# Performance work log

Hardware: AMD Instinct MI355X
Metric: run time of the kernel (lower is better)

## Reference

```python
import jax, jax.numpy as jnp
import numpy as np

BATCH = 8
NDATA = 8192
NPOINT = 1024
NSAMPLE = 32
RADIUS = 0.2
CFEAT = 64


def setup_inputs() -> dict:
    key = jax.random.key(0)
    k1, k2, k3 = jax.random.split(key, 3)
    new_xyz = jax.random.normal(k1, (BATCH, NPOINT, 3), dtype=jnp.float32)
    xyz = jax.random.normal(k2, (BATCH, NDATA, 3), dtype=jnp.float32)
    points = jax.random.normal(k3, (BATCH, NDATA, CFEAT), dtype=jnp.float32)
    return {"new_xyz": new_xyz, "xyz": xyz, "points": points}


def reference(new_xyz, xyz, points):
    # Pairwise distances from every centroid to every dataset point.
    # delta: [B, P, N, 3]
    delta = xyz[:, None, :, :] - new_xyz[:, :, None, :]
    dist = jnp.linalg.norm(delta, axis=-1)  # [B, P, N]

    # Sort by distance (the original does a full argsort per centroid).
    sorted_idx = jnp.argsort(dist, axis=-1).astype(jnp.int32)  # [B, P, N]
    sorted_d = jnp.take_along_axis(dist, sorted_idx, axis=-1)  # [B, P, N]

    # Nearest point index replaces out-of-radius slots.
    nearest = sorted_idx[:, :, 0:1]  # [B, P, 1]
    radius_idx = jnp.where(sorted_d < RADIUS, sorted_idx, nearest)
    idx = radius_idx[:, :, :NSAMPLE]  # [B, P, S] int32 (ndataset >= nsample)

    # Batched gathers: grouped_xyz [B, P, S, 3], grouped_points [B, P, S, C].
    grouped_xyz = jnp.take_along_axis(
        xyz[:, None, :, :], idx[..., None], axis=2)
    grouped_points = jnp.take_along_axis(
        points[:, None, :, :], idx[..., None], axis=2)
    new_points = jnp.concatenate([grouped_xyz, grouped_points], axis=-1)
    return (new_points, idx, grouped_xyz)
```

## Files before the change

### kernel.cpp

```cpp
#include <hip/hip_runtime.h>
#include <math.h>

typedef unsigned int   u32;
typedef unsigned long long u64;

#define BATCH   8
#define NDATA   8192
#define NPOINT  1024
#define NSAMPLE 32
#define CFEAT   64
#define ROWF    67
#define MAXCAND 128
#define QPB     4
#define NB      256

#define OUT_IDX (BATCH*NPOINT*NSAMPLE*ROWF)
#define OUT_GX  (OUT_IDX + BATCH*NPOINT*NSAMPLE)

__device__ __forceinline__ float rnbf(float f) {
    u32 b = __float_as_uint(f);
    b += 0x7FFFu + ((b >> 16) & 1u);
    return __uint_as_float(b & 0xFFFF0000u);
}
__device__ __forceinline__ int clampidx(int v) {
    return (v < 0) ? 0 : (v > NDATA-1 ? NDATA-1 : v);
}
__device__ __forceinline__ int lanes_below(u64 m) {
    return __builtin_amdgcn_mbcnt_hi((u32)(m >> 32),
            __builtin_amdgcn_mbcnt_lo((u32)m, 0));
}
__device__ __forceinline__ int xbucket(float v) {
    int c = (int)floorf((v + 4.5f) * 28.444445f);
    return c < 0 ? 0 : (c > NB-1 ? NB-1 : c);
}

__global__ __launch_bounds__(1024)
void bin_kernel(const float* __restrict__ xyz,
                float4* __restrict__ wp, u32* __restrict__ wst)
{
    __shared__ u32 cnt[NB];
    __shared__ u32 sc[NB];
    const int b = blockIdx.x, tid = threadIdx.x;
    const float* bx = xyz + (size_t)b * NDATA * 3;

    if (tid < NB) cnt[tid] = 0;
    __syncthreads();
    for (int p = tid; p < NDATA; p += 1024)
        atomicAdd(&cnt[xbucket(bx[p*3])], 1u);
    __syncthreads();

    if (tid < NB) sc[tid] = cnt[tid];
    __syncthreads();
    #pragma unroll
    for (int d = 1; d < NB; d <<= 1) {
        u32 t = 0;
        if (tid < NB && tid >= d) t = sc[tid - d];
        __syncthreads();
        if (tid < NB && tid >= d) sc[tid] += t;
        __syncthreads();
    }
    if (tid < NB) {
        u32 excl = (tid == 0) ? 0u : sc[tid - 1];
        cnt[tid] = excl;
        wst[b*(NB+1) + tid] = excl;
        if (tid == 0) wst[b*(NB+1) + NB] = NDATA;
    }
    __syncthreads();

    for (int p = tid; p < NDATA; p += 1024) {
        float x = bx[p*3], y = bx[p*3+1], z = bx[p*3+2];
        u32 pos = atomicAdd(&cnt[xbucket(x)], 1u);
        wp[(size_t)b*NDATA + pos] = make_float4(x, y, z, __uint_as_float((u32)p));
    }
}

__global__ __launch_bounds__(256, 8)
void grouping_kernel(const float* __restrict__ new_xyz,
                     const float* __restrict__ xyz,
                     const float* __restrict__ points,
                     const float4* __restrict__ wp, const u32* __restrict__ wst,
                     float* __restrict__ out, float T)
{
    __shared__ float cand_s[QPB][MAXCAND];
    __shared__ int   cand_i[QPB][MAXCAND];
    __shared__ int   sel[QPB][NSAMPLE];
    __shared__ __align__(16) float st[QPB][8*ROWF];

    const int tid  = threadIdx.x;
    const int wv   = tid >> 6;
    const int lane = tid & 63;
    const int q    = blockIdx.x * QPB + wv;
    const int b    = q >> 10;

    if (lane < NSAMPLE) sel[wv][lane] = 0;

    const float qx = new_xyz[q*3 + 0];
    const float qy = new_xyz[q*3 + 1];
    const float qz = new_xyz[q*3 + 2];
    const float*  bx = xyz + (size_t)b * NDATA * 3;
    const float4* cp = wp  + (size_t)b * NDATA;

    const int blo = xbucket(__fsub_rn(qx, 0.2005f));
    const int bhi = xbucket(__fadd_rn(qx, 0.2005f));
    const u32 j0 = wst[b*(NB+1) + blo];
    const u32 j1 = wst[b*(NB+1) + bhi + 1];

    int n = 0;
    for (u32 jb = j0; jb < j1; jb += 128) {
        u32 ja = jb + lane;
        u32 jc = jb + 64 + lane;
        bool ia = ja < j1;
        bool ib = jc < j1;
        float4 va = cp[ia ? ja : (j1 - 1u)];
        float4 vb = cp[ib ? jc : (j1 - 1u)];
        float dxa = __fsub_rn(va.x, qx);
        float dya = __fsub_rn(va.y, qy);
        float dza = __fsub_rn(va.z, qz);
        float d2a = __fadd_rn(__fadd_rn(__fmul_rn(dxa,dxa), __fmul_rn(dya,dya)),
                              __fmul_rn(dza,dza));
        float dxb = __fsub_rn(vb.x, qx);
        float dyb = __fsub_rn(vb.y, qy);
        float dzb = __fsub_rn(vb.z, qz);
        float d2b = __fadd_rn(__fadd_rn(__fmul_rn(dxb,dxb), __fmul_rn(dyb,dyb)),
                              __fmul_rn(dzb,dzb));
        bool ca = ia && (d2a < T);
        bool cb = ib && (d2b < T);
        u64 ma = __ballot(ca);
        u64 mb = __ballot(cb);
        if (ca) {
            int pos = n + lanes_below(ma);
            if (pos < MAXCAND) {
                cand_s[wv][pos] = __fsqrt_rn(d2a);
                cand_i[wv][pos] = (int)__float_as_uint(va.w);
            }
        }
        n += (int)__popcll(ma);
        if (cb) {
            int pos = n + lanes_below(mb);
            if (pos < MAXCAND) {
                cand_s[wv][pos] = __fsqrt_rn(d2b);
                cand_i[wv][pos] = (int)__float_as_uint(vb.w);
            }
        }
        n += (int)__popcll(mb);
    }

    int mini = 0;
    if (n == 0) {
        float mind = 3.402823466e38f; int mi = 0;
        for (int k = 0; k < NDATA/64; ++k) {
            int i = (k << 6) + lane;
            float dx = __fsub_rn(bx[i*3+0], qx);
            float dy = __fsub_rn(bx[i*3+1], qy);
            float dz = __fsub_rn(bx[i*3+2], qz);
            float d2 = __fadd_rn(__fadd_rn(__fmul_rn(dx,dx), __fmul_rn(dy,dy)),
                                 __fmul_rn(dz,dz));
            if (d2 < mind) { mind = d2; mi = i; }
        }
        float ms = __fsqrt_rn(mind);
        for (int off = 32; off; off >>= 1) {
            float os = __shfl_xor(ms, off);
            int   oi = __shfl_xor(mi, off);
            if (os < ms || (os == ms && oi < mi)) { ms = os; mi = oi; }
        }
        mini = mi;
    }

    __syncthreads();

    const int nj = n > MAXCAND ? MAXCAND : n;
    for (int kk = lane; kk < nj; kk += 64) {
        float sk = cand_s[wv][kk];
        int   ik = cand_i[wv][kk];
        int r = 0;
        for (int mm = 0; mm < nj; ++mm) {
            float sm = cand_s[wv][mm];
            int   im = cand_i[wv][mm];
            r += (int)((sm < sk) | ((sm == sk) & (im < ik)));
        }
        if (r < NSAMPLE) sel[wv][r] = clampidx(ik);
    }
    __syncthreads();
    {
        const int nsel = nj < NSAMPLE ? nj : NSAMPLE;
        if (lane >= nsel && lane < NSAMPLE) {
            int pad = (nj > 0) ? sel[wv][0] : clampidx(mini);
            sel[wv][lane] = pad;
        }
    }
    __syncthreads();

    if (lane < NSAMPLE)
        out[OUT_IDX + (size_t)q*NSAMPLE + lane] = rnbf((float)sel[wv][lane]);

    for (int e = lane; e < NSAMPLE*3; e += 64) {
        int sR = e / 3, c2 = e - sR*3;
        int is = sel[wv][sR];
        out[OUT_GX + (size_t)q*(NSAMPLE*3) + e] = rnbf(bx[is*3 + c2]);
    }

    const float* prow = points + (size_t)b * NDATA * CFEAT;
    float* onp = out + (size_t)q * (NSAMPLE*ROWF);
    const int gq = lane >> 4;
    const int lq = lane & 15;
    for (int g = 0; g < 4; ++g) {
        #pragma unroll
        for (int p = 0; p < 2; ++p) {
            int rl = p*4 + gq;
            int is = sel[wv][g*8 + rl];
            const float4 v = *reinterpret_cast<const float4*>(
                                 prow + (size_t)is*CFEAT + 4*lq);
            float* d = &st[wv][rl*ROWF + 3 + 4*lq];
            d[0] = rnbf(v.x); d[1] = rnbf(v.y); d[2] = rnbf(v.z); d[3] = rnbf(v.w);
        }
        if (lane < 24) {
            int rl = lane / 3, c = lane - rl*3;
            int is = sel[wv][g*8 + rl];
            st[wv][rl*ROWF + c] = rnbf(bx[(size_t)is*3 + c]);
        }
        __syncthreads();
        for (int i = lane; i < 134; i += 64) {
            float4 t = *reinterpret_cast<const float4*>(&st[wv][4*i]);
            *reinterpret_cast<float4*>(onp + (size_t)g*536 + 4*i) = t;
        }
        __syncthreads();
    }
}

extern "C" void kernel_launch(void* const* d_in, const int* in_sizes, int n_in,
                              void* d_out, int out_size, void* d_ws, size_t ws_size,
                              hipStream_t stream) {
    union { u32 u; float f; } lo, hi, mid;
    lo.u = 0u; hi.f = 0.05f;
    while (hi.u - lo.u > 1u) {
        mid.u = lo.u + (hi.u - lo.u) / 2u;
        if (sqrtf(mid.f) >= 0.2f) hi.u = mid.u; else lo.u = mid.u;
    }
    float T = hi.f;

    float4* wp  = (float4*)d_ws;
    u32*    wst = (u32*)(wp + (size_t)BATCH*NDATA);

    const float* nxz = (const float*)d_in[0];
    const float* xyz = (const float*)d_in[1];
    const float* pts = (const float*)d_in[2];

    bin_kernel<<<BATCH, 1024, 0, stream>>>(xyz, wp, wst);
    grouping_kernel<<<(BATCH*NPOINT)/QPB, 256, 0, stream>>>(
        nxz, xyz, pts, wp, wst, (float*)d_out, T);
}
```

Baseline: 126.1 us.

## Split binning into parallel count/scan/scatter kernels and drop block barriers

The single eight-block binning kernel becomes three kernels. A 64-block histogram count writes partial histograms, a single-block scan builds global bucket offsets, and a 64-block scatter places points into their buckets with global atomics. The goal is to spread the binning work over far more compute units than eight blocks can use. In the grouping kernel, every block-wide barrier is replaced by a compiler-only memory fence, since each wave touches only its own shared-memory slice. This relies on in-order LDS access within a wave, and it adds two extra kernel launches plus nondeterministic ordering of points within a bucket.

Result: slower. 131.4 us (+4.2%).

```diff
diff --git a/kernel.cpp b/kernel.cpp
--- a/kernel.cpp
+++ b/kernel.cpp
@@ -13,6 +13,7 @@
 #define MAXCAND 128
 #define QPB     4
 #define NB      256
+#define NCH     8
 
 #define OUT_IDX (BATCH*NPOINT*NSAMPLE*ROWF)
 #define OUT_GX  (OUT_IDX + BATCH*NPOINT*NSAMPLE)
@@ -29,47 +30,78 @@
     return __builtin_amdgcn_mbcnt_hi((u32)(m >> 32),
             __builtin_amdgcn_mbcnt_lo((u32)m, 0));
 }
+__device__ __forceinline__ void wave_lds_fence() {
+    asm volatile("" ::: "memory");
+}
 __device__ __forceinline__ int xbucket(float v) {
     int c = (int)floorf((v + 4.5f) * 28.444445f);
     return c < 0 ? 0 : (c > NB-1 ? NB-1 : c);
 }
 
+__global__ __launch_bounds__(256)
+void count_kernel(const float* __restrict__ xyz, u32* __restrict__ part)
+{
+    __shared__ u32 hist[NB];
+    const int b = blockIdx.x >> 3, c = blockIdx.x & 7, tid = threadIdx.x;
+    hist[tid] = 0;
+    __syncthreads();
+    const float* bx = xyz + (size_t)b * NDATA * 3;
+    #pragma unroll
+    for (int k = 0; k < 4; ++k) {
+        int p = c*1024 + k*256 + tid;
+        atomicAdd(&hist[xbucket(bx[p*3])], 1u);
+    }
+    __syncthreads();
+    part[(size_t)(b*NCH + c)*NB + tid] = hist[tid];
+}
+
 __global__ __launch_bounds__(1024)
-void bin_kernel(const float* __restrict__ xyz,
-                float4* __restrict__ wp, u32* __restrict__ wst)
-{
-    __shared__ u32 cnt[NB];
-    __shared__ u32 sc[NB];
-    const int b = blockIdx.x, tid = threadIdx.x;
+void scan_kernel(const u32* __restrict__ part,
+                 u32* __restrict__ wst, u32* __restrict__ gcur)
+{
+    __shared__ u32 sc[BATCH*NB];
+    const int tid = threadIdx.x;
+    #pragma unroll
+    for (int h = 0; h < 2; ++h) {
+        int e = tid + h*1024;
+        int bb = e >> 8, i = e & 255;
+        u32 s = 0;
+        for (int c = 0; c < NCH; ++c) s += part[(size_t)(bb*NCH + c)*NB + i];
+        sc[e] = s;
+    }
+    __syncthreads();
+    #pragma unroll
+    for (int d = 1; d < NB; d <<= 1) {
+        u32 t0 = 0, t1 = 0;
+        if ((tid & 255) >= d)          t0 = sc[tid - d];
+        if (((tid+1024) & 255) >= d)   t1 = sc[tid + 1024 - d];
+        __syncthreads();
+        if ((tid & 255) >= d)          sc[tid]        += t0;
+        if (((tid+1024) & 255) >= d)   sc[tid + 1024] += t1;
+        __syncthreads();
+    }
+    #pragma unroll
+    for (int h = 0; h < 2; ++h) {
+        int e = tid + h*1024;
+        int bb = e >> 8, i = e & 255;
+        u32 excl = (i == 0) ? 0u : sc[e - 1];
+        wst[bb*(NB+1) + i] = excl;
+        gcur[bb*NB + i]    = excl;
+        if (i == 0) wst[bb*(NB+1) + NB] = NDATA;
+    }
+}
+
+__global__ __launch_bounds__(256)
+void scatter_kernel(const float* __restrict__ xyz,
+                    u32* __restrict__ gcur, float4* __restrict__ wp)
+{
+    const int b = blockIdx.x >> 3, c = blockIdx.x & 7, tid = threadIdx.x;
     const float* bx = xyz + (size_t)b * NDATA * 3;
-
-    if (tid < NB) cnt[tid] = 0;
-    __syncthreads();
-    for (int p = tid; p < NDATA; p += 1024)
-        atomicAdd(&cnt[xbucket(bx[p*3])], 1u);
-    __syncthreads();
-
-    if (tid < NB) sc[tid] = cnt[tid];
-    __syncthreads();
-    #pragma unroll
-    for (int d = 1; d < NB; d <<= 1) {
-        u32 t = 0;
-        if (tid < NB && tid >= d) t = sc[tid - d];
-        __syncthreads();
-        if (tid < NB && tid >= d) sc[tid] += t;
-        __syncthreads();
-    }
-    if (tid < NB) {
-        u32 excl = (tid == 0) ? 0u : sc[tid - 1];
-        cnt[tid] = excl;
-        wst[b*(NB+1) + tid] = excl;
-        if (tid == 0) wst[b*(NB+1) + NB] = NDATA;
-    }
-    __syncthreads();
-
-    for (int p = tid; p < NDATA; p += 1024) {
+    #pragma unroll
+    for (int k = 0; k < 4; ++k) {
+        int p = c*1024 + k*256 + tid;
         float x = bx[p*3], y = bx[p*3+1], z = bx[p*3+2];
-        u32 pos = atomicAdd(&cnt[xbucket(x)], 1u);
+        u32 pos = atomicAdd(&gcur[b*NB + xbucket(x)], 1u);
         wp[(size_t)b*NDATA + pos] = make_float4(x, y, z, __uint_as_float((u32)p));
     }
 }
@@ -166,7 +198,7 @@
         mini = mi;
     }
 
-    __syncthreads();
+    wave_lds_fence();
 
     const int nj = n > MAXCAND ? MAXCAND : n;
     for (int kk = lane; kk < nj; kk += 64) {
@@ -180,7 +212,7 @@
         }
         if (r < NSAMPLE) sel[wv][r] = clampidx(ik);
     }
-    __syncthreads();
+    wave_lds_fence();
     {
         const int nsel = nj < NSAMPLE ? nj : NSAMPLE;
         if (lane >= nsel && lane < NSAMPLE) {
@@ -188,7 +220,7 @@
             sel[wv][lane] = pad;
         }
     }
-    __syncthreads();
+    wave_lds_fence();
 
     if (lane < NSAMPLE)
         out[OUT_IDX + (size_t)q*NSAMPLE + lane] = rnbf((float)sel[wv][lane]);
@@ -218,12 +250,12 @@
             int is = sel[wv][g*8 + rl];
             st[wv][rl*ROWF + c] = rnbf(bx[(size_t)is*3 + c]);
         }
-        __syncthreads();
+        wave_lds_fence();
         for (int i = lane; i < 134; i += 64) {
             float4 t = *reinterpret_cast<const float4*>(&st[wv][4*i]);
             *reinterpret_cast<float4*>(onp + (size_t)g*536 + 4*i) = t;
         }
-        __syncthreads();
+        wave_lds_fence();
     }
 }
 
@@ -238,14 +270,18 @@
     }
     float T = hi.f;
 
-    float4* wp  = (float4*)d_ws;
-    u32*    wst = (u32*)(wp + (size_t)BATCH*NDATA);
+    float4* wp   = (float4*)d_ws;
+    u32*    wst  = (u32*)(wp + (size_t)BATCH*NDATA);
+    u32*    gcur = wst + BATCH*(NB+1);
+    u32*    part = gcur + BATCH*NB;
 
     const float* nxz = (const float*)d_in[0];
     const float* xyz = (const float*)d_in[1];
     const float* pts = (const float*)d_in[2];
 
-    bin_kernel<<<BATCH, 1024, 0, stream>>>(xyz, wp, wst);
+    count_kernel  <<<BATCH*NCH, 256,  0, stream>>>(xyz, part);
+    scan_kernel   <<<1,         1024, 0, stream>>>(part, wst, gcur);
+    scatter_kernel<<<BATCH*NCH, 256,  0, stream>>>(xyz, gcur, wp);
     grouping_kernel<<<(BATCH*NPOINT)/QPB, 256, 0, stream>>>(
         nxz, xyz, pts, wp, wst, (float*)d_out, T);
 }
```

## Bin points on a 2D x-y grid to shrink the radius candidate scan

Applied to the files above, without the earlier changes.

Replaces the 256-bucket 1D x-slab binning with a 32x32 grid keyed on x and y, sorted so that y-cells within an x column are contiguous. Each query now scans only the y-range within each overlapping x column, which reads far fewer points than a full x-slab. The prefix scan in the binning kernel is rewritten with wave shuffles instead of a barrier-heavy shared-memory scan. In exchange, the coarser cells (about 0.28 wide against a 0.2 radius) mean several column segments per query, and the scan loop drops from two loads per iteration to one.

After: 123.2 us (median of 2 runs). -2.3%, faster.

```diff
diff --git a/kernel.cpp b/kernel.cpp
--- a/kernel.cpp
+++ b/kernel.cpp
@@ -12,7 +12,9 @@
 #define ROWF    67
 #define MAXCAND 128
 #define QPB     4
-#define NB      256
+#define NBX     32
+#define NBY     32
+#define NBK     (NBX*NBY)
 
 #define OUT_IDX (BATCH*NPOINT*NSAMPLE*ROWF)
 #define OUT_GX  (OUT_IDX + BATCH*NPOINT*NSAMPLE)
@@ -29,47 +31,58 @@
     return __builtin_amdgcn_mbcnt_hi((u32)(m >> 32),
             __builtin_amdgcn_mbcnt_lo((u32)m, 0));
 }
-__device__ __forceinline__ int xbucket(float v) {
-    int c = (int)floorf((v + 4.5f) * 28.444445f);
-    return c < 0 ? 0 : (c > NB-1 ? NB-1 : c);
+__device__ __forceinline__ int cbucket(float v) {
+    int c = (int)floorf((v + 4.5f) * 3.5555556f);
+    return c < 0 ? 0 : (c > NBX-1 ? NBX-1 : c);
+}
+__device__ __forceinline__ int key2(float x, float y) {
+    return cbucket(x)*NBY + cbucket(y);
 }
 
 __global__ __launch_bounds__(1024)
 void bin_kernel(const float* __restrict__ xyz,
                 float4* __restrict__ wp, u32* __restrict__ wst)
 {
-    __shared__ u32 cnt[NB];
-    __shared__ u32 sc[NB];
+    __shared__ u32 cnt[NBK];
+    __shared__ u32 wsum[16];
     const int b = blockIdx.x, tid = threadIdx.x;
+    const int lane = tid & 63, wv = tid >> 6;
     const float* bx = xyz + (size_t)b * NDATA * 3;
 
-    if (tid < NB) cnt[tid] = 0;
+    cnt[tid] = 0;
     __syncthreads();
     for (int p = tid; p < NDATA; p += 1024)
-        atomicAdd(&cnt[xbucket(bx[p*3])], 1u);
-    __syncthreads();
-
-    if (tid < NB) sc[tid] = cnt[tid];
-    __syncthreads();
+        atomicAdd(&cnt[key2(bx[p*3], bx[p*3+1])], 1u);
+    __syncthreads();
+
+    u32 v = cnt[tid];
+    u32 s = v;
     #pragma unroll
-    for (int d = 1; d < NB; d <<= 1) {
-        u32 t = 0;
-        if (tid < NB && tid >= d) t = sc[tid - d];
-        __syncthreads();
-        if (tid < NB && tid >= d) sc[tid] += t;
-        __syncthreads();
-    }
-    if (tid < NB) {
-        u32 excl = (tid == 0) ? 0u : sc[tid - 1];
-        cnt[tid] = excl;
-        wst[b*(NB+1) + tid] = excl;
-        if (tid == 0) wst[b*(NB+1) + NB] = NDATA;
-    }
+    for (int off = 1; off < 64; off <<= 1) {
+        u32 t = __shfl_up(s, off);
+        if (lane >= off) s += t;
+    }
+    if (lane == 63) wsum[wv] = s;
+    __syncthreads();
+    if (tid < 16) {
+        u32 w = wsum[tid];
+        #pragma unroll
+        for (int off = 1; off < 16; off <<= 1) {
+            u32 t = __shfl_up(w, off);
+            if (tid >= off) w += t;
+        }
+        wsum[tid] = w;
+    }
+    __syncthreads();
+    u32 excl = s - v + (wv ? wsum[wv-1] : 0u);
+    wst[b*(NBK+1) + tid] = excl;
+    cnt[tid] = excl;
+    if (tid == 0) wst[b*(NBK+1) + NBK] = NDATA;
     __syncthreads();
 
     for (int p = tid; p < NDATA; p += 1024) {
         float x = bx[p*3], y = bx[p*3+1], z = bx[p*3+2];
-        u32 pos = atomicAdd(&cnt[xbucket(x)], 1u);
+        u32 pos = atomicAdd(&cnt[key2(x, y)], 1u);
         wp[(size_t)b*NDATA + pos] = make_float4(x, y, z, __uint_as_float((u32)p));
     }
 }
@@ -100,49 +113,37 @@
     const float*  bx = xyz + (size_t)b * NDATA * 3;
     const float4* cp = wp  + (size_t)b * NDATA;
 
-    const int blo = xbucket(__fsub_rn(qx, 0.2005f));
-    const int bhi = xbucket(__fadd_rn(qx, 0.2005f));
-    const u32 j0 = wst[b*(NB+1) + blo];
-    const u32 j1 = wst[b*(NB+1) + bhi + 1];
+    const int bxlo = cbucket(__fsub_rn(qx, 0.2005f));
+    const int bxhi = cbucket(__fadd_rn(qx, 0.2005f));
+    const int bylo = cbucket(__fsub_rn(qy, 0.2005f));
+    const int byhi = cbucket(__fadd_rn(qy, 0.2005f));
+    const u32* ws = wst + b*(NBK+1);
 
     int n = 0;
-    for (u32 jb = j0; jb < j1; jb += 128) {
-        u32 ja = jb + lane;
-        u32 jc = jb + 64 + lane;
-        bool ia = ja < j1;
-        bool ib = jc < j1;
-        float4 va = cp[ia ? ja : (j1 - 1u)];
-        float4 vb = cp[ib ? jc : (j1 - 1u)];
-        float dxa = __fsub_rn(va.x, qx);
-        float dya = __fsub_rn(va.y, qy);
-        float dza = __fsub_rn(va.z, qz);
-        float d2a = __fadd_rn(__fadd_rn(__fmul_rn(dxa,dxa), __fmul_rn(dya,dya)),
-                              __fmul_rn(dza,dza));
-        float dxb = __fsub_rn(vb.x, qx);
-        float dyb = __fsub_rn(vb.y, qy);
-        float dzb = __fsub_rn(vb.z, qz);
-        float d2b = __fadd_rn(__fadd_rn(__fmul_rn(dxb,dxb), __fmul_rn(dyb,dyb)),
-                              __fmul_rn(dzb,dzb));
-        bool ca = ia && (d2a < T);
-        bool cb = ib && (d2b < T);
-        u64 ma = __ballot(ca);
-        u64 mb = __ballot(cb);
-        if (ca) {
-            int pos = n + lanes_below(ma);
-            if (pos < MAXCAND) {
-                cand_s[wv][pos] = __fsqrt_rn(d2a);
-                cand_i[wv][pos] = (int)__float_as_uint(va.w);
+    for (int c = bxlo; c <= bxhi; ++c) {
+        const u32 j0 = ws[c*NBY + bylo];
+        const u32 j1 = ws[c*NBY + byhi + 1];
+        for (u32 jb = j0; jb < j1; jb += 64) {
+            u32 j  = jb + lane;
+            bool in = j < j1;
+            u32 jj = in ? j : (j1 - 1u);
+            float4 vv = cp[jj];
+            float dx = __fsub_rn(vv.x, qx);
+            float dy = __fsub_rn(vv.y, qy);
+            float dz = __fsub_rn(vv.z, qz);
+            float d2 = __fadd_rn(__fadd_rn(__fmul_rn(dx,dx), __fmul_rn(dy,dy)),
+                                 __fmul_rn(dz,dz));
+            bool cc = in && (d2 < T);
+            u64 m = __ballot(cc);
+            if (cc) {
+                int pos = n + lanes_below(m);
+                if (pos < MAXCAND) {
+                    cand_s[wv][pos] = __fsqrt_rn(d2);
+                    cand_i[wv][pos] = (int)__float_as_uint(vv.w);
+                }
             }
-        }
-        n += (int)__popcll(ma);
-        if (cb) {
-            int pos = n + lanes_below(mb);
-            if (pos < MAXCAND) {
-                cand_s[wv][pos] = __fsqrt_rn(d2b);
-                cand_i[wv][pos] = (int)__float_as_uint(vb.w);
-            }
-        }
-        n += (int)__popcll(mb);
+            n += (int)__popcll(m);
+        }
     }
 
     int mini = 0;
```
